# Kernel tuning notes

Measured on AMD Instinct MI355X. Metric: run time of the kernel, lower is better.

## Reference

```python
import jax, jax.numpy as jnp
import numpy as np

B, L, N, D, TOPK, OUT_V = 32, 512, 1024, 64, 20, 1024
BN_EPS = 1e-5
NEG_SLOPE = 0.2


def setup_inputs() -> dict:
    key = jax.random.key(0)
    ks = jax.random.split(key, 8)
    s = lambda k, shape, sc=0.05: jax.random.normal(k, shape, jnp.float32) * sc
    return {
        "x_enc": jax.random.normal(ks[0], (B, L, N), jnp.float32),
        "emb": s(ks[1], (N, D), 0.1),          # nn.Embedding(variate, d_model).weight
        "lin_W": s(ks[2], (L, D)),              # GraphLayer.lin (no bias)
        "att_i": s(ks[3], (D,)),
        "att_j": s(ks[4], (D,)),
        "att_em_i": s(ks[5], (D,)),
        "att_em_j": s(ks[6], (D,)),
        "gnn_b": jnp.zeros((D,), jnp.float32),  # GraphLayer bias (concat=False)
        "g1": jnp.ones((D,), jnp.float32), "b1": jnp.zeros((D,), jnp.float32),   # GNNLayer.bn
        "g2": jnp.ones((D,), jnp.float32), "b2": jnp.zeros((D,), jnp.float32),   # bn_outlayer_in
        "out_W": s(ks[7], (D, 1)), "out_b": jnp.zeros((1,), jnp.float32),        # OutLayer Linear(d_model, 1)
    }


def _forward(x_enc, emb, lin_W, att_i, att_j, att_em_i, att_em_j,
             gnn_b, g1, b1, g2, b2, out_W, out_b):
    # --- LIN: LayerNorm(input_len, eps=0, no affine) over time, first OUT_V variates ---
    xv = jnp.transpose(x_enc[:, :, :OUT_V], (0, 2, 1))          # [B, OUT_V, L]
    xv = (xv - xv.mean(-1, keepdims=True)) / jnp.sqrt(xv.var(-1, keepdims=True))
    x_enc = x_enc.at[:, :, :OUT_V].set(jnp.transpose(xv, (0, 2, 1)))
    x_enc = jnp.nan_to_num(x_enc, nan=0.0, posinf=0.0, neginf=0.0)

    gt = x_enc[:, -1:, :OUT_V]                                   # [B, 1, OUT_V]
    enc = x_enc.at[:, -1:, :OUT_V].set(0.0)

    # x = enc.transpose(0,1).view(-1, L)  (faithful to original reshape)
    x = jnp.transpose(enc, (1, 0, 2)).reshape(-1, L)             # [B*N, L]

    # --- dynamic top-k cosine-similarity graph (embeddings detached) ---
    w = jax.lax.stop_gradient(emb)
    nrm = jnp.linalg.norm(w, axis=-1)
    cos = (w @ w.T) / (nrm[:, None] * nrm[None, :])              # [N, N]
    topk_idx = jax.lax.top_k(cos, TOPK)[1]                       # [N, TOPK]
    src = topk_idx.reshape(-1)                                   # gated_j (source)
    dst = jnp.repeat(jnp.arange(N), TOPK)                        # gated_i (target)

    offs = (jnp.arange(B) * N)[:, None]
    src_b = (src[None, :] + offs).reshape(-1)                    # [B*N*TOPK]
    dst_b = (dst[None, :] + offs).reshape(-1)

    # remove_self_loops (mask out) then add_self_loops for all B*N nodes
    num_nodes = B * N
    self_mask = jnp.concatenate([src_b == dst_b, jnp.zeros(num_nodes, bool)])
    src_all = jnp.concatenate([src_b, jnp.arange(num_nodes)])
    dst_all = jnp.concatenate([dst_b, jnp.arange(num_nodes)])

    # --- GraphLayer (GAT-style, heads=1, concat=False) ---
    h = x @ lin_W                                                # [B*N, D]
    all_emb = jnp.tile(emb, (B, 1))                              # [B*N, D]

    logit = (h[dst_all] @ att_i + all_emb[dst_all] @ att_em_i
             + h[src_all] @ att_j + all_emb[src_all] @ att_em_j)  # [E]
    logit = jnp.where(logit >= 0, logit, NEG_SLOPE * logit)      # leaky_relu(0.2)
    logit = jnp.where(self_mask, -jnp.inf, logit)

    seg_max = jax.ops.segment_max(logit, dst_all, num_segments=num_nodes)
    expv = jnp.where(self_mask, 0.0, jnp.exp(logit - seg_max[dst_all]))
    denom = jax.ops.segment_sum(expv, dst_all, num_segments=num_nodes)
    alpha = expv / denom[dst_all]

    out = jax.ops.segment_sum(h[src_all] * alpha[:, None], dst_all,
                              num_segments=num_nodes) + gnn_b    # [B*N, D]

    # GNNLayer: BatchNorm1d(D) (batch stats) + ReLU
    out = (out - out.mean(0)) / jnp.sqrt(out.var(0) + BN_EPS) * g1 + b1
    out = jax.nn.relu(out)

    # --- combine with embedding, bn_outlayer_in, OutLayer ---
    xg = out.reshape(B, N, D) * emb[None]                        # [B, N, D]
    xg = jnp.transpose(xg, (0, 2, 1))                            # [B, D, N]
    mu = xg.mean((0, 2), keepdims=True)
    var = xg.var((0, 2), keepdims=True)
    xg = (xg - mu) / jnp.sqrt(var + BN_EPS) * g2[None, :, None] + b2[None, :, None]
    xg = jnp.transpose(jax.nn.relu(xg), (0, 2, 1))               # [B, N, D]

    o = xg @ out_W + out_b                                       # [B, N, 1]
    o = jnp.transpose(o, (0, 2, 1))                              # [B, 1, N]
    return o[:, :, :OUT_V], gt


def reference(x_enc, emb, lin_W, att_i, att_j, att_em_i, att_em_j,
              gnn_b, g1, b1, g2, b2, out_W, out_b):
    return _forward(x_enc, emb, lin_W, att_i, att_j, att_em_i, att_em_j,
                    gnn_b, g1, b1, g2, b2, out_W, out_b)
```

## Files before the change

### kernel.cpp

```cpp
#include <hip/hip_runtime.h>
#include <stdint.h>

#define BB 32
#define LL 512
#define NNODES 1024
#define DD 64
#define TOPK 20
#define NTOT (BB*NNODES)
#define LNSZ (LL*NNODES)

typedef short short8 __attribute__((ext_vector_type(8)));
typedef float floatx4 __attribute__((ext_vector_type(4)));

__device__ __forceinline__ float bf2f(unsigned short u){
    union { unsigned int i; float f; } x; x.i = ((unsigned int)u) << 16; return x.f;
}
__device__ __forceinline__ unsigned short f2bf(float f){
    union { float f; unsigned int i; } x; x.f = f;
    unsigned int u = x.i;
    return (unsigned short)((u + 0x7FFFu + ((u >> 16) & 1u)) >> 16);
}
__device__ __forceinline__ void unpack2(unsigned int w, float& lo, float& hi){
    union { unsigned int i; float f; } a, b;
    a.i = w << 16; b.i = w & 0xFFFF0000u;
    lo = a.f; hi = b.f;
}
__device__ __forceinline__ float ldf(const void* p, int i, int isf){
    return isf ? ((const float*)p)[i] : bf2f(((const unsigned short*)p)[i]);
}
__device__ __forceinline__ int detect_isf(const void* xv){
    const unsigned short* x = (const unsigned short*)xv;
    int lane = threadIdx.x & 63;
    unsigned int idx = ((unsigned)lane * 131071u) & 0x7FFFFFu;
    float v = bf2f(x[idx * 2]);
    float a = fabsf(v);
    int crazy = (!(a <= 1e3f)) || (v != 0.f && a < 1e-6f);
    unsigned long long m = __ballot(crazy);
    return __popcll(m) > 16;
}

__global__ void __launch_bounds__(256) k01_prep(const void* x, const void* lw, unsigned short* wt,
                                                const void* emb, const void* aemi, const void* aemj,
                                                float* eai, float* eaj, float* embT, float* rsqm,
                                                float* part, float* stats){
    int isf = detect_isf(x);
    int t = threadIdx.x;
    if (blockIdx.x == 0) stats[t] = 0.f;
    if (blockIdx.x < 128){
        int id = blockIdx.x * 256 + t;
        int k = id >> 6, d = id & 63;
        unsigned short w = isf ? f2bf(((const float*)lw)[id]) : ((const unsigned short*)lw)[id];
        wt[d * 512 + k] = w;
        {
            int j = id;
            int dd = j >> 10, m = j & 1023;
            embT[j] = ldf(emb, m * 64 + dd, isf);
            j = id + 32768;
            dd = j >> 10; m = j & 1023;
            embT[j] = ldf(emb, m * 64 + dd, isf);
        }
        if (id < 1024){
            int n = id;
            float s1 = 0.f, s2 = 0.f;
            for (int dd = 0; dd < 64; dd++){
                float e = ldf(emb, n * 64 + dd, isf);
                s1 += e * ldf(aemi, dd, isf);
                s2 += e * ldf(aemj, dd, isf);
            }
            eai[n] = s1; eaj[n] = s2;
            float sq = 0.f;
            if (!isf){
                const uint4* pm = (const uint4*)((const unsigned short*)emb + n * 64);
                #pragma unroll
                for (int i = 0; i < 8; i++){
                    uint4 ww = pm[i];
                    float a0,a1,a2,a3,a4,a5,a6,a7;
                    unpack2(ww.x,a0,a1); unpack2(ww.y,a2,a3); unpack2(ww.z,a4,a5); unpack2(ww.w,a6,a7);
                    sq += a0*a0 + a1*a1 + a2*a2 + a3*a3 + a4*a4 + a5*a5 + a6*a6 + a7*a7;
                }
            } else {
                const float4* pm = (const float4*)((const float*)emb + n * 64);
                #pragma unroll
                for (int i = 0; i < 16; i++){
                    float4 ww = pm[i];
                    sq += ww.x*ww.x + ww.y*ww.y + ww.z*ww.z + ww.w*ww.w;
                }
            }
            rsqm[n] = rsqrtf(sq);
        }
    }
    int b = blockIdx.x >> 5, lq = blockIdx.x & 31;
    int th = t & 127, rh = t >> 7;
    int n0 = th * 8;
    int l0 = lq * 16 + rh * 8;
    size_t base = (size_t)b * LNSZ + (size_t)l0 * NNODES + n0;
    float s0=0,s1=0,s2=0,s3=0,s4=0,s5=0,s6=0,s7=0;
    float q0=0,q1=0,q2=0,q3=0,q4=0,q5=0,q6=0,q7=0;
    if (isf){
        const float* p = (const float*)x + base;
        #pragma unroll
        for (int i = 0; i < 8; i++){
            float4 wa = *(const float4*)p;
            float4 wb = *(const float4*)(p + 4);
            s0+=wa.x; q0+=wa.x*wa.x; s1+=wa.y; q1+=wa.y*wa.y;
            s2+=wa.z; q2+=wa.z*wa.z; s3+=wa.w; q3+=wa.w*wa.w;
            s4+=wb.x; q4+=wb.x*wb.x; s5+=wb.y; q5+=wb.y*wb.y;
            s6+=wb.z; q6+=wb.z*wb.z; s7+=wb.w; q7+=wb.w*wb.w;
            p += NNODES;
        }
    } else {
        const unsigned short* p = (const unsigned short*)x + base;
        #pragma unroll
        for (int i = 0; i < 8; i++){
            uint4 w = *(const uint4*)p;
            float e0,e1,e2,e3,e4,e5,e6,e7;
            unpack2(w.x,e0,e1); unpack2(w.y,e2,e3); unpack2(w.z,e4,e5); unpack2(w.w,e6,e7);
            s0+=e0; q0+=e0*e0; s1+=e1; q1+=e1*e1;
            s2+=e2; q2+=e2*e2; s3+=e3; q3+=e3*e3;
            s4+=e4; q4+=e4*e4; s5+=e5; q5+=e5*e5;
            s6+=e6; q6+=e6*e6; s7+=e7; q7+=e7*e7;
            p += NNODES;
        }
    }
    int pidx = lq * 2 + rh;
    int v = b * 1024 + n0;
    float2* pp = (float2*)part + (size_t)pidx * 32768 + v;
    pp[0]=make_float2(s0,q0); pp[1]=make_float2(s1,q1);
    pp[2]=make_float2(s2,q2); pp[3]=make_float2(s3,q3);
    pp[4]=make_float2(s4,q4); pp[5]=make_float2(s5,q5);
    pp[6]=make_float2(s6,q6); pp[7]=make_float2(s7,q7);
}

__global__ void __launch_bounds__(256) k13_topk(const void* emb, const float* embT, const float* rsqm,
                                                int* topk, const void* x, const float* part,
                                                float* mr, float* outp){
    __shared__ float enf[64];
    __shared__ float n2s;
    __shared__ float crow[1024];
    int isf = detect_isf(x);
    int wave = threadIdx.x >> 6, lane = threadIdx.x & 63;
    int n = blockIdx.x;
    if (blockIdx.x < 128){
        int v = blockIdx.x * 256 + threadIdx.x;
        float s = 0.f, q = 0.f;
        for (int i = 0; i < 64; i++){
            float2 w = ((const float2*)part)[(size_t)i * 32768 + v];
            s += w.x; q += w.y;
        }
        float mean = s * (1.f/512.f);
        float var  = q * (1.f/512.f) - mean * mean;
        float rstd = var > 0.f ? rsqrtf(var) : 0.f;
        ((float2*)mr)[v] = make_float2(mean, rstd);
        int b = v >> 10, nn = v & 1023;
        float xv = ldf(x, (int)((size_t)b * LNSZ + (size_t)511 * NNODES + nn), isf);
        outp[NTOT + v] = (xv - mean) * rstd;
    }
    if (wave == 0){
        float e = ldf(emb, n * 64 + lane, isf);
        enf[lane] = e;
        float p1 = e * e;
        #pragma unroll
        for (int m = 1; m < 64; m <<= 1) p1 += __shfl_xor(p1, m, 64);
        if (lane == 0) n2s = p1;
    }
    __syncthreads();
    float rn_own = rsqrtf(n2s);
    const float* en = enf;
    int mb = wave * 256 + lane * 4;
    float dot0 = 0.f, dot1 = 0.f, dot2 = 0.f, dot3 = 0.f;
    if (!isf){
        #pragma unroll
        for (int i = 0; i < 8; i++){
            float4 a0 = *(const float4*)(embT + (i*8+0)*1024 + mb);
            float4 a1 = *(const float4*)(embT + (i*8+1)*1024 + mb);
            float4 a2 = *(const float4*)(embT + (i*8+2)*1024 + mb);
            float4 a3 = *(const float4*)(embT + (i*8+3)*1024 + mb);
            float4 a4 = *(const float4*)(embT + (i*8+4)*1024 + mb);
            float4 a5 = *(const float4*)(embT + (i*8+5)*1024 + mb);
            float4 a6 = *(const float4*)(embT + (i*8+6)*1024 + mb);
            float4 a7 = *(const float4*)(embT + (i*8+7)*1024 + mb);
            const float* e8 = en + i * 8;
            dot0 += e8[0]*a0.x + e8[1]*a1.x + e8[2]*a2.x + e8[3]*a3.x
                  + e8[4]*a4.x + e8[5]*a5.x + e8[6]*a6.x + e8[7]*a7.x;
            dot1 += e8[0]*a0.y + e8[1]*a1.y + e8[2]*a2.y + e8[3]*a3.y
                  + e8[4]*a4.y + e8[5]*a5.y + e8[6]*a6.y + e8[7]*a7.y;
            dot2 += e8[0]*a0.z + e8[1]*a1.z + e8[2]*a2.z + e8[3]*a3.z
                  + e8[4]*a4.z + e8[5]*a5.z + e8[6]*a6.z + e8[7]*a7.z;
            dot3 += e8[0]*a0.w + e8[1]*a1.w + e8[2]*a2.w + e8[3]*a3.w
                  + e8[4]*a4.w + e8[5]*a5.w + e8[6]*a6.w + e8[7]*a7.w;
        }
    } else {
        #pragma unroll
        for (int i = 0; i < 16; i++){
            float4 a0 = *(const float4*)(embT + (i*4+0)*1024 + mb);
            float4 a1 = *(const float4*)(embT + (i*4+1)*1024 + mb);
            float4 a2 = *(const float4*)(embT + (i*4+2)*1024 + mb);
            float4 a3 = *(const float4*)(embT + (i*4+3)*1024 + mb);
            const float* e4 = en + i * 4;
            dot0 += e4[0]*a0.x + e4[1]*a1.x + e4[2]*a2.x + e4[3]*a3.x;
            dot1 += e4[0]*a0.y + e4[1]*a1.y + e4[2]*a2.y + e4[3]*a3.y;
            dot2 += e4[0]*a0.z + e4[1]*a1.z + e4[2]*a2.z + e4[3]*a3.z;
            dot3 += e4[0]*a0.w + e4[1]*a1.w + e4[2]*a2.w + e4[3]*a3.w;
        }
    }
    crow[mb+0] = dot0 * rn_own * rsqm[mb+0];
    crow[mb+1] = dot1 * rn_own * rsqm[mb+1];
    crow[mb+2] = dot2 * rn_own * rsqm[mb+2];
    crow[mb+3] = dot3 * rn_own * rsqm[mb+3];
    __syncthreads();
    if (wave != 0) return;
    float va[16];
    #pragma unroll
    for (int ii = 0; ii < 16; ii++) va[ii] = crow[ii * 64 + lane];
    for (int k = 0; k < TOPK; k++){
        float t8[8]; int x8[8];
        #pragma unroll
        for (int j = 0; j < 8; j++){
            bool c = va[2*j+1] > va[2*j];
            t8[j] = c ? va[2*j+1] : va[2*j]; x8[j] = c ? 2*j+1 : 2*j;
        }
        #pragma unroll
        for (int j = 0; j < 4; j++){
            bool c = t8[2*j+1] > t8[2*j];
            t8[j] = c ? t8[2*j+1] : t8[2*j]; x8[j] = c ? x8[2*j+1] : x8[2*j];
        }
        #pragma unroll
        for (int j = 0; j < 2; j++){
            bool c = t8[2*j+1] > t8[2*j];
            t8[j] = c ? t8[2*j+1] : t8[2*j]; x8[j] = c ? x8[2*j+1] : x8[2*j];
        }
        bool c0 = t8[1] > t8[0];
        float bv = c0 ? t8[1] : t8[0]; int bi = c0 ? x8[1] : x8[0];
        int bm = bi * 64 + lane;
        #pragma unroll
        for (int s = 1; s < 64; s <<= 1){
            float ov = __shfl_xor(bv, s, 64);
            int   om = __shfl_xor(bm, s, 64);
            bool u = (ov > bv) || (ov == bv && om < bm);
            bv = u ? ov : bv; bm = u ? om : bm;
        }
        if (lane == 0) topk[n * TOPK + k] = bm;
        int evi = bm >> 6;
        bool own = ((bm & 63) == lane);
        #pragma unroll
        for (int ii = 0; ii < 16; ii++)
            va[ii] = (own && ii == evi) ? -__builtin_inff() : va[ii];
    }
}

__global__ void __launch_bounds__(256) k2_gemm_h(const void* x, const unsigned short* wt,
                                                const float* mr, unsigned short* hb,
                                                const void* atti, const void* attj,
                                                const float* eai, const float* eaj,
                                                float* ai, float* aj){
    __shared__ uint4 A4[64 * 16];
    __shared__ uint4 W4[64 * 16];
    __shared__ float4 colp4[256];
    int isf = detect_isf(x);
    int t = threadIdx.x;
    int q = blockIdx.x & 63, mtile = blockIdx.x >> 6;
    int b = q >> 1, nbase = (q & 1) * 512;
    size_t xbase = (size_t)b * LNSZ + nbase;

    colp4[t] = ((const float4*)mr)[q * 256 + t];

    int wave = t >> 6, lane = t & 63;
    int quad = lane >> 4, lcol = lane & 15;
    floatx4 acc[4];
    for (int j = 0; j < 4; j++) acc[j] = (floatx4){0.f,0.f,0.f,0.f};
    __syncthreads();

    for (int kc = 0; kc < 4; kc++){
        #pragma unroll
        for (int i = 0; i < 4; i++){
            int id = i * 256 + t;
            int l = id >> 4, c16 = id & 15;
            int lg = mtile * 64 + l;
            uint4 o;
            if (lg == 511){
                o = make_uint4(0u, 0u, 0u, 0u);
            } else {
                size_t ofs = xbase + (size_t)lg * NNODES + kc * 128 + c16 * 8;
                float e0,e1,e2,e3,e4,e5,e6,e7;
                if (isf){
                    const float4* px = (const float4*)((const float*)x + ofs);
                    float4 wa = px[0], wb = px[1];
                    e0=wa.x; e1=wa.y; e2=wa.z; e3=wa.w; e4=wb.x; e5=wb.y; e6=wb.z; e7=wb.w;
                } else {
                    uint4 w = *(const uint4*)((const unsigned short*)x + ofs);
                    unpack2(w.x,e0,e1); unpack2(w.y,e2,e3); unpack2(w.z,e4,e5); unpack2(w.w,e6,e7);
                }
                int f4b = kc * 64 + c16 * 4;
                float4 pA = colp4[f4b+0], pB = colp4[f4b+1], pC = colp4[f4b+2], pD = colp4[f4b+3];
                e0 = (e0 - pA.x) * pA.y;  e1 = (e1 - pA.z) * pA.w;
                e2 = (e2 - pB.x) * pB.y;  e3 = (e3 - pB.z) * pB.w;
                e4 = (e4 - pC.x) * pC.y;  e5 = (e5 - pC.z) * pC.w;
                e6 = (e6 - pD.x) * pD.y;  e7 = (e7 - pD.z) * pD.w;
                o.x = (unsigned)f2bf(e0) | ((unsigned)f2bf(e1) << 16);
                o.y = (unsigned)f2bf(e2) | ((unsigned)f2bf(e3) << 16);
                o.z = (unsigned)f2bf(e4) | ((unsigned)f2bf(e5) << 16);
                o.w = (unsigned)f2bf(e6) | ((unsigned)f2bf(e7) << 16);
            }
            A4[l * 16 + (c16 ^ (l & 15))] = o;
        }
        #pragma unroll
        for (int i = 0; i < 4; i++){
            int id = i * 256 + t;
            int dd = id >> 4, c16 = id & 15;
            uint4 w = *(const uint4*)(wt + dd * 512 + kc * 128 + c16 * 8);
            W4[dd * 16 + (c16 ^ (dd & 15))] = w;
        }
        __syncthreads();
        #pragma unroll
        for (int ks = 0; ks < 4; ks++){
            int cx = ks * 4 + quad;
            int arow = wave * 16 + lcol;
            short8 af = *(const short8*)&A4[arow * 16 + (cx ^ lcol)];
            short8 bfr[4];
            #pragma unroll
            for (int tc = 0; tc < 4; tc++)
                bfr[tc] = *(const short8*)&W4[(tc * 16 + lcol) * 16 + (cx ^ lcol)];
            #pragma unroll
            for (int tc = 0; tc < 4; tc++)
                acc[tc] = __builtin_amdgcn_mfma_f32_16x16x32_bf16(af, bfr[tc], acc[tc], 0, 0, 0);
        }
        __syncthreads();
    }
    float aw[4], jw[4];
    #pragma unroll
    for (int tc = 0; tc < 4; tc++){
        int dcol = tc * 16 + lcol;
        aw[tc] = ldf(atti, dcol, isf);
        jw[tc] = ldf(attj, dcol, isf);
    }
    #pragma unroll
    for (int r = 0; r < 4; r++){
        float pi = 0.f, pj = 0.f;
        #pragma unroll
        for (int tc = 0; tc < 4; tc++){
            float hv = acc[tc][r];
            pi += hv * aw[tc];
            pj += hv * jw[tc];
        }
        #pragma unroll
        for (int s = 1; s < 16; s <<= 1){
            pi += __shfl_xor(pi, s, 64);
            pj += __shfl_xor(pj, s, 64);
        }
        if (lcol == 0){
            int lrow = wave * 16 + quad * 4 + r;
            int row = (mtile * 64 + lrow) * 64 + q;
            int n = row & 1023;
            ai[row] = pi + eai[n];
            aj[row] = pj + eaj[n];
        }
    }
    #pragma unroll
    for (int tc = 0; tc < 4; tc++){
        int dcol = tc * 16 + lcol;
        #pragma unroll
        for (int r = 0; r < 4; r++){
            int lrow = wave * 16 + quad * 4 + r;
            int row = (mtile * 64 + lrow) * 64 + q;
            hb[(size_t)row * 64 + dcol] = f2bf(acc[tc][r]);
        }
    }
}

__global__ void __launch_bounds__(256) k5_attn(const unsigned short* hb, const float* ai, const float* aj,
                                               const int* topk, const void* gnn_b, float* out, const void* x){
    int isf = detect_isf(x);
    int wave = threadIdx.x >> 6, lane = threadIdx.x & 63;
    float gb = ldf(gnn_b, lane, isf);
    int v = blockIdx.x * 4 + wave;
    int n = v & 1023, bbase = v & ~1023;
    int srcv; bool valid;
    if (lane < TOPK){
        int id = topk[n * TOPK + lane];
        srcv = bbase | id;
        valid = (id != n);
    } else if (lane == TOPK){
        srcv = v; valid = true;
    } else { srcv = v; valid = false; }
    float l = ai[v] + aj[srcv];
    l = (l >= 0.f) ? l : 0.2f * l;
    if (!valid) l = -__builtin_inff();
    float m = l;
    #pragma unroll
    for (int s = 1; s < 64; s <<= 1){ float o = __shfl_xor(m, s, 64); m = fmaxf(m, o); }
    float ev = valid ? __expf(l - m) : 0.f;
    float dsum = ev;
    #pragma unroll
    for (int s = 1; s < 64; s <<= 1) dsum += __shfl_xor(dsum, s, 64);
    float rd = 1.f / dsum;
    float acc = 0.f;
    #pragma unroll
    for (int j = 0; j <= TOPK; j++){
        float e = __shfl(ev, j, 64);
        int  sj = __shfl(srcv, j, 64);
        acc += e * bf2f(hb[(size_t)sj * 64 + lane]);
    }
    out[(size_t)v * 64 + lane] = acc * rd + gb;
}

__global__ void __launch_bounds__(256) k5b_stats(const float* out, float* stats1){
    __shared__ float bs[256], bq[256];
    int wave = threadIdx.x >> 6, lane = threadIdx.x & 63;
    int v0 = blockIdx.x * 128 + wave * 32;
    float ssum = 0.f, ssq = 0.f;
    for (int i = 0; i < 32; i++){
        float x = out[(size_t)(v0 + i) * 64 + lane];
        ssum += x; ssq += x * x;
    }
    bs[threadIdx.x] = ssum; bq[threadIdx.x] = ssq;
    __syncthreads();
    if (wave == 0){
        float s  = bs[lane] + bs[64+lane] + bs[128+lane] + bs[192+lane];
        float qq = bq[lane] + bq[64+lane] + bq[128+lane] + bq[192+lane];
        atomicAdd(&stats1[lane], s);
        atomicAdd(&stats1[64 + lane], qq);
    }
}

__global__ void __launch_bounds__(256) k6_stats2(const float* out, const float* stats1, const void* g1,
                                                 const void* b1, const void* emb,
                                                 float* stats2, const void* x){
    __shared__ float bs[256], bq[256];
    int isf = detect_isf(x);
    int wave = threadIdx.x >> 6, lane = threadIdx.x & 63;
    float mu   = stats1[lane] * (1.f/32768.f);
    float var  = stats1[64 + lane] * (1.f/32768.f) - mu * mu;
    float rstd = 1.f / sqrtf(var + 1e-5f);
    float g = ldf(g1, lane, isf), bb = ldf(b1, lane, isf);
    float ssum = 0.f, ssq = 0.f;
    int v0 = (blockIdx.x * 4 + wave) * 16;
    for (int i = 0; i < 16; i++){
        int v = v0 + i; int n = v & 1023;
        float xv = out[(size_t)v * 64 + lane];
        float y = fmaxf((xv - mu) * rstd * g + bb, 0.f);
        float z = y * ldf(emb, n * 64 + lane, isf);
        ssum += z; ssq += z * z;
    }
    bs[threadIdx.x] = ssum; bq[threadIdx.x] = ssq;
    __syncthreads();
    if (wave == 0){
        float s  = bs[lane] + bs[64+lane] + bs[128+lane] + bs[192+lane];
        float qq = bq[lane] + bq[64+lane] + bq[128+lane] + bq[192+lane];
        atomicAdd(&stats2[lane], s);
        atomicAdd(&stats2[64 + lane], qq);
    }
}

__global__ void __launch_bounds__(256) k7_out(const float* out, const float* stats1, const float* stats2,
                                              const void* g1, const void* b1,
                                              const void* g2, const void* b2,
                                              const void* emb, const void* outw,
                                              const void* outb, float* o, const void* x){
    int isf = detect_isf(x);
    int wave = threadIdx.x >> 6, lane = threadIdx.x & 63;
    float mu1   = stats1[lane] * (1.f/32768.f);
    float var1  = stats1[64 + lane] * (1.f/32768.f) - mu1 * mu1;
    float rstd1 = 1.f / sqrtf(var1 + 1e-5f);
    float g1v = ldf(g1, lane, isf), b1v = ldf(b1, lane, isf);
    float mu2   = stats2[lane] * (1.f/32768.f);
    float var2  = stats2[64 + lane] * (1.f/32768.f) - mu2 * mu2;
    float rstd2 = 1.f / sqrtf(var2 + 1e-5f);
    float g2v = ldf(g2, lane, isf), b2v = ldf(b2, lane, isf);
    float w = ldf(outw, lane, isf);
    float ob = ldf(outb, 0, isf);
    int v0 = (blockIdx.x * 4 + wave) * 16;
    for (int i = 0; i < 16; i++){
        int v = v0 + i; int n = v & 1023;
        float xv = out[(size_t)v * 64 + lane];
        float z = fmaxf((xv - mu1) * rstd1 * g1v + b1v, 0.f) * ldf(emb, n * 64 + lane, isf);
        float y = fmaxf((z - mu2) * rstd2 * g2v + b2v, 0.f);
        float p = y * w;
        for (int s = 1; s < 64; s <<= 1) p += __shfl_xor(p, s, 64);
        if (lane == 0) o[v] = p + ob;
    }
}

extern "C" void kernel_launch(void* const* d_in, const int* in_sizes, int n_in,
                              void* d_out, int out_size, void* d_ws, size_t ws_size,
                              hipStream_t stream){
    const void* x    = d_in[0];
    const void* emb  = d_in[1];
    const void* linW = d_in[2];
    const void* atti = d_in[3];
    const void* attj = d_in[4];
    const void* aemi = d_in[5];
    const void* aemj = d_in[6];
    const void* gnnb = d_in[7];
    const void* g1   = d_in[8];
    const void* b1   = d_in[9];
    const void* g2   = d_in[10];
    const void* b2   = d_in[11];
    const void* outw = d_in[12];
    const void* outb = d_in[13];
    float* o = (float*)d_out;

    char* w = (char*)d_ws;
    float*          mr    = (float*)(w + 0);
    unsigned short* wt    = (unsigned short*)(w + 262144);
    unsigned short* hb    = (unsigned short*)(w + 327680);
    float*          eai   = (float*)(w + 8716288);
    float*          eaj   = (float*)(w + 8720384);
    int*            topk  = (int*)(w + 8724480);
    float*          ai    = (float*)(w + 8806400);
    float*          aj    = (float*)(w + 8937472);
    float*          outg  = (float*)(w + 9068544);
    float*          embT  = (float*)(w + 13262848);
    float*          rsqm  = (float*)(w + 13524992);
    float*          stats = (float*)(w + 17457152);
    float*          part  = (float*)(w + 18874368);

    hipLaunchKernelGGL(k01_prep, dim3(1024), dim3(256), 0, stream, x, linW, wt, emb, aemi, aemj,
                       eai, eaj, embT, rsqm, part, stats);
    hipLaunchKernelGGL(k13_topk, dim3(1024), dim3(256), 0, stream, emb, embT, rsqm, topk, x, part, mr, o);
    hipLaunchKernelGGL(k2_gemm_h, dim3(512), dim3(256), 0, stream, x, wt, mr, hb, atti, attj, eai, eaj, ai, aj);
    hipLaunchKernelGGL(k5_attn,  dim3(8192), dim3(256), 0, stream, hb, ai, aj, topk, gnnb, outg, x);
    hipLaunchKernelGGL(k5b_stats, dim3(256), dim3(256), 0, stream, outg, stats);
    hipLaunchKernelGGL(k6_stats2, dim3(512), dim3(256), 0, stream, outg, stats, g1, b1, emb, stats + 128, x);
    hipLaunchKernelGGL(k7_out,   dim3(512),  dim3(256), 0, stream, outg, stats, stats + 128,
                       g1, b1, g2, b2, emb, outw, outb, o, x);
}
```

Before: 237.5 us.

## Shrink GEMM M-tile to 16 rows and split D columns across waves

The h=x·W GEMM kernel now takes 16-row tiles instead of 64, so it launches 2048 blocks instead of 512. Each wave computes one 16-column slice of D rather than all 64 columns, and the attention dot products are combined across waves through a small shared-memory reduction. The aim is to raise occupancy and parallelism across the GPU's compute units. The cost is that each block reloads the full W tile for a quarter of the rows, which means more redundant W traffic and an extra barrier.

```diff
diff --git a/kernel.cpp b/kernel.cpp
--- a/kernel.cpp
+++ b/kernel.cpp
@@ -253,9 +253,10 @@
                                                 const void* atti, const void* attj,
                                                 const float* eai, const float* eaj,
                                                 float* ai, float* aj){
-    __shared__ uint4 A4[64 * 16];
+    __shared__ uint4 A4[16 * 16];
     __shared__ uint4 W4[64 * 16];
     __shared__ float4 colp4[256];
+    __shared__ float red[4][16][2];
     int isf = detect_isf(x);
     int t = threadIdx.x;
     int q = blockIdx.x & 63, mtile = blockIdx.x >> 6;
@@ -266,16 +267,13 @@
 
     int wave = t >> 6, lane = t & 63;
     int quad = lane >> 4, lcol = lane & 15;
-    floatx4 acc[4];
-    for (int j = 0; j < 4; j++) acc[j] = (floatx4){0.f,0.f,0.f,0.f};
+    floatx4 acc = (floatx4){0.f,0.f,0.f,0.f};
     __syncthreads();
 
     for (int kc = 0; kc < 4; kc++){
-        #pragma unroll
-        for (int i = 0; i < 4; i++){
-            int id = i * 256 + t;
-            int l = id >> 4, c16 = id & 15;
-            int lg = mtile * 64 + l;
+        {
+            int l = t >> 4, c16 = t & 15;
+            int lg = mtile * 16 + l;
             uint4 o;
             if (lg == 511){
                 o = make_uint4(0u, 0u, 0u, 0u);
@@ -301,7 +299,7 @@
                 o.z = (unsigned)f2bf(e4) | ((unsigned)f2bf(e5) << 16);
                 o.w = (unsigned)f2bf(e6) | ((unsigned)f2bf(e7) << 16);
             }
-            A4[l * 16 + (c16 ^ (l & 15))] = o;
+            A4[l * 16 + (c16 ^ l)] = o;
         }
         #pragma unroll
         for (int i = 0; i < 4; i++){
@@ -314,56 +312,42 @@
         #pragma unroll
         for (int ks = 0; ks < 4; ks++){
             int cx = ks * 4 + quad;
-            int arow = wave * 16 + lcol;
-            short8 af = *(const short8*)&A4[arow * 16 + (cx ^ lcol)];
-            short8 bfr[4];
-            #pragma unroll
-            for (int tc = 0; tc < 4; tc++)
-                bfr[tc] = *(const short8*)&W4[(tc * 16 + lcol) * 16 + (cx ^ lcol)];
-            #pragma unroll
-            for (int tc = 0; tc < 4; tc++)
-                acc[tc] = __builtin_amdgcn_mfma_f32_16x16x32_bf16(af, bfr[tc], acc[tc], 0, 0, 0);
+            short8 af  = *(const short8*)&A4[lcol * 16 + (cx ^ lcol)];
+            short8 bfr = *(const short8*)&W4[(wave * 16 + lcol) * 16 + (cx ^ lcol)];
+            acc = __builtin_amdgcn_mfma_f32_16x16x32_bf16(af, bfr, acc, 0, 0, 0);
         }
         __syncthreads();
     }
-    float aw[4], jw[4];
-    #pragma unroll
-    for (int tc = 0; tc < 4; tc++){
-        int dcol = tc * 16 + lcol;
-        aw[tc] = ldf(atti, dcol, isf);
-        jw[tc] = ldf(attj, dcol, isf);
-    }
+    float awv = ldf(atti, wave * 16 + lcol, isf);
+    float jwv = ldf(attj, wave * 16 + lcol, isf);
     #pragma unroll
     for (int r = 0; r < 4; r++){
-        float pi = 0.f, pj = 0.f;
-        #pragma unroll
-        for (int tc = 0; tc < 4; tc++){
-            float hv = acc[tc][r];
-            pi += hv * aw[tc];
-            pj += hv * jw[tc];
-        }
+        float pi = acc[r] * awv;
+        float pj = acc[r] * jwv;
         #pragma unroll
         for (int s = 1; s < 16; s <<= 1){
             pi += __shfl_xor(pi, s, 64);
             pj += __shfl_xor(pj, s, 64);
         }
         if (lcol == 0){
-            int lrow = wave * 16 + quad * 4 + r;
-            int row = (mtile * 64 + lrow) * 64 + q;
-            int n = row & 1023;
-            ai[row] = pi + eai[n];
-            aj[row] = pj + eaj[n];
-        }
+            red[wave][quad * 4 + r][0] = pi;
+            red[wave][quad * 4 + r][1] = pj;
+        }
+    }
+    __syncthreads();
+    if (t < 16){
+        int row = t;
+        float pi = red[0][row][0] + red[1][row][0] + red[2][row][0] + red[3][row][0];
+        float pj = red[0][row][1] + red[1][row][1] + red[2][row][1] + red[3][row][1];
+        int rg = (mtile * 16 + row) * 64 + q;
+        int n = rg & 1023;
+        ai[rg] = pi + eai[n];
+        aj[rg] = pj + eaj[n];
     }
     #pragma unroll
-    for (int tc = 0; tc < 4; tc++){
-        int dcol = tc * 16 + lcol;
-        #pragma unroll
-        for (int r = 0; r < 4; r++){
-            int lrow = wave * 16 + quad * 4 + r;
-            int row = (mtile * 64 + lrow) * 64 + q;
-            hb[(size_t)row * 64 + dcol] = f2bf(acc[tc][r]);
-        }
+    for (int r = 0; r < 4; r++){
+        int rg = (mtile * 16 + quad * 4 + r) * 64 + q;
+        hb[(size_t)rg * 64 + wave * 16 + lcol] = f2bf(acc[r]);
     }
 }
 
@@ -517,7 +501,7 @@
     hipLaunchKernelGGL(k01_prep, dim3(1024), dim3(256), 0, stream, x, linW, wt, emb, aemi, aemj,
                        eai, eaj, embT, rsqm, part, stats);
     hipLaunchKernelGGL(k13_topk, dim3(1024), dim3(256), 0, stream, emb, embT, rsqm, topk, x, part, mr, o);
-    hipLaunchKernelGGL(k2_gemm_h, dim3(512), dim3(256), 0, stream, x, wt, mr, hb, atti, attj, eai, eaj, ai, aj);
+    hipLaunchKernelGGL(k2_gemm_h, dim3(2048), dim3(256), 0, stream, x, wt, mr, hb, atti, attj, eai, eaj, ai, aj);
     hipLaunchKernelGGL(k5_attn,  dim3(8192), dim3(256), 0, stream, hb, ai, aj, topk, gnnb, outg, x);
     hipLaunchKernelGGL(k5b_stats, dim3(256), dim3(256), 0, stream, outg, stats);
     hipLaunchKernelGGL(k6_stats2, dim3(512), dim3(256), 0, stream, outg, stats, g1, b1, emb, stats + 128, x);
```

Result: no change. 236.3 us (-0.5%).
